# Kernel tuning notes

Hardware: AMD Instinct MI355X
Metric: run time of the kernel (lower is better)

The kernel has to match this reference:

```python
import jax, jax.numpy as jnp
import numpy as np

# FlowNetC correlation hyperparameters (from init_kwargs)
PAD = 20
KS = 1
MD = 20
S1 = 1
S2 = 2
MUL = 1


def setup_inputs() -> dict:
    key = jax.random.key(0)
    k1, k2 = jax.random.split(key)
    B, C, H, W = 8, 256, 96, 128
    input1 = jax.random.normal(k1, (B, C, H, W), dtype=jnp.float32)
    input2 = jax.random.normal(k2, (B, C, H, W), dtype=jnp.float32)
    return {"input1": input1, "input2": input2}


def _correlation(in1, in2):
    b, c, h, w = in1.shape
    p1 = jnp.pad(in1, ((0, 0), (0, 0), (PAD, PAD), (PAD, PAD)))
    p2 = jnp.pad(in2, ((0, 0), (0, 0), (PAD, PAD), (PAD, PAD)))
    hp, wp = h + 2 * PAD, w + 2 * PAD
    out_h = (hp - 2 * MD - KS) // S1 + 1
    out_w = (wp - 2 * MD - KS) // S1 + 1
    d = 2 * MD // S2 + 1  # number of displacement steps per axis (21)

    # fixed center region of input1: [b, c, out_h, out_w]
    region1 = p1[:, :, MD:MD + out_h * S1:S1, MD:MD + out_w * S1:S1]

    offs = (jnp.arange(d) - d // 2) * S2  # displacement offsets
    dys, dxs = jnp.meshgrid(offs, offs, indexing='ij')
    dys = dys.reshape(-1)
    dxs = dxs.reshape(-1)

    def step(carry, dydx):
        dy, dx = dydx
        y0 = MD + dy
        x0 = MD + dx
        valid = (y0 >= 0) & (x0 >= 0) & (y0 + out_h * S1 <= hp) & (x0 + out_w * S1 <= wp)
        reg2 = jax.lax.dynamic_slice(
            p2, (0, 0, y0, x0), (b, c, out_h * S1, out_w * S1)
        )[:, :, ::S1, ::S1]
        corr = (region1 * reg2).sum(axis=1) * MUL  # [b, out_h, out_w]
        corr = jnp.where(valid, corr, jnp.zeros_like(corr))
        return carry, corr

    _, chans = jax.lax.scan(step, None, (dys, dxs))  # [d*d, b, out_h, out_w]
    return jnp.transpose(chans, (1, 0, 2, 3))  # [b, d*d, out_h, out_w]


def reference(input1, input2):
    return _correlation(input1, input2)
```

## Files before the change

kernel.cpp:

```cpp
#include <hip/hip_runtime.h>
#include <stdint.h>

#define B_N   8
#define C_N   256
#define H_N   96
#define W_N   128
#define NCK   8
#define ND    21
#define NK    (ND * ND)

typedef __attribute__((ext_vector_type(8))) short short8;
typedef __attribute__((ext_vector_type(4))) float f32x4;

__device__ __forceinline__ uint32_t f2bf(float f) {
  uint32_t u = __builtin_bit_cast(uint32_t, f);
  return (u + 0x7fffu + ((u >> 16) & 1u)) >> 16;
}
__device__ __forceinline__ uint32_t packbf(float lo, float hi) {
  return f2bf(lo) | (f2bf(hi) << 16);
}
__device__ __forceinline__ void async16(void* lds_dst, const void* gsrc) {
  __builtin_amdgcn_global_load_lds(
      (const __attribute__((address_space(1))) void*)gsrc,
      (__attribute__((address_space(3))) void*)lds_dst, 16, 0, 0);
}

__global__ __launch_bounds__(256) void prep(const float* __restrict__ in1,
                                            const float* __restrict__ in2,
                                            unsigned short* __restrict__ Apre,
                                            unsigned short* __restrict__ Bpre) {
  __shared__ float tile[32][W_N + 1];
  int blk = blockIdx.x;
  bool isA = blk < 6144;
  int rblk = isA ? blk : blk - 6144;
  int ck = rblk & 7, bi = rblk >> 3;
  int b = bi / H_N, row = bi % H_N;
  const float* src = (isA ? in1 : in2) + ((size_t)(b * C_N + ck * 32) * H_N + row) * W_N;
  int tid = threadIdx.x;
  for (int idx = tid; idx < 32 * W_N; idx += 256) {
    int c = idx >> 7, j = idx & 127;
    tile[c][j] = src[(size_t)c * (H_N * W_N) + j];
  }
  __syncthreads();
  if (isA) {
    uint32_t* dst = (uint32_t*)Apre + (size_t)rblk * 2048;
    for (int q = tid; q < 2048; q += 256) {
      int e2 = q & 3, ln = (q >> 2) & 63, tp = q >> 8;
      int t = tp >> 1, p = tp & 1;
      int m = ln & 15, kg = ln >> 4;
      int c0 = kg * 8 + 2 * e2;
      int j = 32 * t + 2 * m + p;
      dst[q] = packbf(tile[c0][j], tile[c0 + 1][j]);
    }
  } else {
    uint32_t* dst = (uint32_t*)Bpre + (size_t)rblk * 3072;
    for (int q = tid; q < 3072; q += 256) {
      int e2 = q & 3, ln = (q >> 2) & 63, sp = q >> 8;
      int s = sp >> 1, p = sp & 1;
      int m = ln & 15, kg = ln >> 4;
      int c0 = kg * 8 + 2 * e2;
      int x = 32 * s + 2 * m - 20 + p;
      dst[q] = ((unsigned)x < 128u) ? packbf(tile[c0][x], tile[c0 + 1][x]) : 0u;
    }
  }
}

__global__ __launch_bounds__(768, 3) void corr_main(const unsigned short* __restrict__ Apre,
                                                    const unsigned short* __restrict__ Bpre,
                                                    float* __restrict__ out) {
  __shared__ __align__(16) char Bl[2][36864];

  int h = blockIdx.x;
  int b = h & 7, blk = h >> 3;
  int Y, pos;
  if (blk < 18)       { Y = blk - 20;                pos = 0; }
  else if (blk < 54)  { int t = blk - 18;  Y = -2 + (t >> 1); pos = t & 1; }
  else if (blk < 234) { int t = blk - 54;  Y = 16 + t / 3;    pos = t % 3; }
  else if (blk < 270) { int t = blk - 234; Y = 76 + (t >> 1); pos = t & 1; }
  else                { Y = 94 + (blk - 270);        pos = 0; }
  int g_min = (Y > 75) ? (Y - 70) / 6 : 0;
  int g_max = (Y + 20) / 6; if (g_max > 6) g_max = 6;

  int tid = threadIdx.x;
  int lane = tid & 63, w = tid >> 6;
  int rr = w >> 2, sub = w & 3;
  int p = sub & 1, th = sub >> 1;
  int m = lane & 15, kg = lane >> 4;

  int gidx = g_min + pos * 3 + rr;
  bool act = gidx <= g_max;
  int i_el = Y + 20 - 6 * gidx;
  int dyb = 3 * gidx;

  const char* bsrc[3];
  bool yval[3];
#pragma unroll
  for (int k = 0; k < 3; ++k) {
    int y = Y + 2 * k;
    yval[k] = (unsigned)y < (unsigned)H_N;
    bsrc[k] = (const char*)Bpre + (size_t)((b * H_N + (yval[k] ? y : 0)) * NCK) * 12288
              + w * 1024 + lane * 16;
  }
#pragma unroll
  for (int k = 0; k < 3; ++k) {
    if (!yval[k]) {
      short8 z = {};
      *(short8*)(&Bl[0][0] + k * 12288 + w * 1024 + lane * 16) = z;
      *(short8*)(&Bl[1][0] + k * 12288 + w * 1024 + lane * 16) = z;
    }
  }

  f32x4 acc[2][3][3];
#pragma unroll
  for (int a0i = 0; a0i < 2; ++a0i)
#pragma unroll
    for (int a1i = 0; a1i < 3; ++a1i)
#pragma unroll
      for (int a2i = 0; a2i < 3; ++a2i) acc[a0i][a1i][a2i] = {0.f, 0.f, 0.f, 0.f};

  const char* Ap = (const char*)Apre + (size_t)(b * H_N + (act ? i_el : 0)) * 65536
                   + ((4 * th + p) << 10) + lane * 16;

#pragma unroll
  for (int k = 0; k < 3; ++k)
    if (yval[k]) async16(&Bl[0][0] + k * 12288 + w * 1024, bsrc[k]);
  __syncthreads();

  for (int ck = 0; ck < NCK; ++ck) {
    char* cur = &Bl[ck & 1][0];
    if (ck < NCK - 1) {
      char* nxt = &Bl[(ck + 1) & 1][0];
#pragma unroll
      for (int k = 0; k < 3; ++k)
        if (yval[k]) async16(nxt + k * 12288 + w * 1024, bsrc[k] + (size_t)(ck + 1) * 12288);
    }
    if (act) {
      short8 a0 = *(const short8*)(Ap);
      short8 a1 = *(const short8*)(Ap + 2048);
#pragma unroll
      for (int ss = 0; ss < 4; ++ss) {
        int s = 2 * th + ss;
#pragma unroll
        for (int g = 0; g < 3; ++g) {
          short8 bbv = *(const short8*)(cur + g * 12288 + ((2 * s + p) << 10) + lane * 16);
          if (ss <= 2) acc[0][g][ss]     = __builtin_amdgcn_mfma_f32_16x16x32_bf16(a0, bbv, acc[0][g][ss], 0, 0, 0);
          if (ss >= 1) acc[1][g][ss - 1] = __builtin_amdgcn_mfma_f32_16x16x32_bf16(a1, bbv, acc[1][g][ss - 1], 0, 0, 0);
        }
      }
    }
    Ap += 8192;
    __syncthreads();
  }

  float* outl = (float*)(&Bl[0][0] + rr * 11072);
  int gt = sub * 64 + lane;
#pragma unroll
  for (int g = 0; g < 3; ++g) {
    if (act) {
#pragma unroll
      for (int tt = 0; tt < 2; ++tt) {
        int t = 2 * th + tt;
#pragma unroll
        for (int dl = 0; dl < 3; ++dl) {
#pragma unroll
          for (int r = 0; r < 4; ++r) {
            int a_ = kg * 4 + r;
            int dxi = 16 * dl + m - a_;
            if (dxi >= 0 && dxi <= 20) {
              int j = 2 * (16 * t + a_) + p;
              outl[dxi * 129 + j] = acc[tt][g][dl][r];
            }
          }
        }
      }
    }
    __syncthreads();
    if (act) {
      int dyi = dyb + g;
      size_t obase = ((size_t)(b * NK + dyi * ND) * H_N + i_el) * W_N;
      for (int idx = gt; idx < ND * W_N; idx += 256) {
        int dxi = idx >> 7, j = idx & 127;
        out[obase + (size_t)dxi * (H_N * W_N) + j] = outl[dxi * 129 + j];
      }
    }
    __syncthreads();
  }
}

__global__ void corr_naive(const float* __restrict__ in1, const float* __restrict__ in2,
                           float* __restrict__ out) {
  size_t o = (size_t)blockIdx.x * 256 + threadIdx.x;
  const size_t total = (size_t)B_N * NK * H_N * W_N;
  if (o >= total) return;
  int j = o & 127;
  int i = (int)((o >> 7) % H_N);
  int k = (int)((o / ((size_t)H_N * W_N)) % NK);
  int b = (int)(o / ((size_t)NK * H_N * W_N));
  int dyi = k / ND, dxi = k % ND;
  int y = i + 2 * dyi - 20, x = j + 2 * dxi - 20;
  float s = 0.f;
  if ((unsigned)y < (unsigned)H_N && (unsigned)x < (unsigned)W_N) {
    const float* p1 = in1 + ((size_t)b * C_N * H_N + i) * W_N + j;
    const float* p2 = in2 + ((size_t)b * C_N * H_N + y) * W_N + x;
    for (int c = 0; c < C_N; ++c)
      s += p1[(size_t)c * H_N * W_N] * p2[(size_t)c * H_N * W_N];
  }
  out[o] = s;
}

extern "C" void kernel_launch(void* const* d_in, const int* in_sizes, int n_in,
                              void* d_out, int out_size, void* d_ws, size_t ws_size,
                              hipStream_t stream) {
  const float* in1 = (const float*)d_in[0];
  const float* in2 = (const float*)d_in[1];
  float* out = (float*)d_out;

  const size_t A_BYTES = (size_t)6144 * 8192;
  const size_t B_BYTES = (size_t)6144 * 12288;
  if (ws_size < A_BYTES + B_BYTES) {
    size_t total = (size_t)B_N * NK * H_N * W_N;
    corr_naive<<<(int)((total + 255) / 256), 256, 0, stream>>>(in1, in2, out);
    return;
  }
  unsigned short* Apre = (unsigned short*)d_ws;
  unsigned short* Bpre = (unsigned short*)((char*)d_ws + A_BYTES);

  prep<<<12288, 256, 0, stream>>>(in1, in2, Apre, Bpre);
  corr_main<<<2304, 768, 0, stream>>>(Apre, Bpre, out);
}
```

Baseline: 200.4 us.

## Restructure correlation main loop into manually pipelined register/LDS double-buffered schedule

Rewrites the channel-chunk loop of corr_main as a fully unrolled software pipeline. A and edge B fragments are loaded straight into registers one chunk ahead, and only the 6 shared inner B units per row are staged in LDS through async loads. Explicit vmcnt waits, sched_barriers and raw s_barriers replace __syncthreads. This is meant to shrink the LDS footprint and overlap global loads with MFMA work, at the cost of more registers and fragile hand-written wait counts.

```diff
diff --git a/kernel.cpp b/kernel.cpp
--- a/kernel.cpp
+++ b/kernel.cpp
@@ -65,10 +65,60 @@
   }
 }
 
+#define MF(a, b, c) __builtin_amdgcn_mfma_f32_16x16x32_bf16(a, b, c, 0, 0, 0)
+#define SB0() __builtin_amdgcn_sched_barrier(0)
+#define BAR() __builtin_amdgcn_s_barrier()
+#define WAITV7() asm volatile("s_waitcnt vmcnt(7)" ::: "memory")
+#define WAITV0() asm volatile("s_waitcnt vmcnt(0)" ::: "memory")
+
+#define MF6(A0, A1, S0, S1, S2, S3, GI) do {                    \
+  acc[0][GI][0] = MF(A0, S0, acc[0][GI][0]);                    \
+  acc[0][GI][1] = MF(A0, S1, acc[0][GI][1]);                    \
+  acc[1][GI][0] = MF(A1, S1, acc[1][GI][0]);                    \
+  acc[0][GI][2] = MF(A0, S2, acc[0][GI][2]);                    \
+  acc[1][GI][1] = MF(A1, S2, acc[1][GI][1]);                    \
+  acc[1][GI][2] = MF(A1, S3, acc[1][GI][2]);                    \
+} while (0)
+
+#define ISSUE(AV0, AV1, GV0, GV1, GV2, CK) do {                                   \
+  async16(lds + (((CK) & 1) ? dst0b1 : dst0b0), src0 + (size_t)(CK) * 12288);     \
+  async16(lds + (((CK) & 1) ? dst1b1 : dst1b0), src1 + (size_t)(CK) * 12288);     \
+  AV0 = *(const short8*)(Ap + (size_t)(CK) * 8192);                               \
+  AV1 = *(const short8*)(Ap + (size_t)(CK) * 8192 + 2048);                        \
+  GV0 = *(const short8*)(bg0 + (size_t)(CK) * 12288);                             \
+  GV1 = *(const short8*)(bg1 + (size_t)(CK) * 12288);                             \
+  GV2 = *(const short8*)(bg2 + (size_t)(CK) * 12288);                             \
+} while (0)
+
+#define COMPG(AV0, AV1, GV, YV, GI, CK) do {                                      \
+  const char* cb_ = lds + ((CK) & 1) * 24576 + dsb + (GI) * 8192;                 \
+  short8 q0 = *(const short8*)(cb_);                                              \
+  short8 q1 = *(const short8*)(cb_ + 2048);                                       \
+  short8 q2 = *(const short8*)(cb_ + 4096);                                       \
+  short8 eg = (YV) ? (GV) : z8;                                                   \
+  if (th == 0) { MF6(AV0, AV1, eg, q0, q1, q2, GI); }                             \
+  else         { MF6(AV0, AV1, q0, q1, q2, eg, GI); }                             \
+} while (0)
+
+#define COMP(AV0, AV1, GV0, GV1, GV2, CK) do {                                    \
+  if (act) {                                                                      \
+    COMPG(AV0, AV1, GV0, yv0, 0, CK);                                             \
+    COMPG(AV0, AV1, GV1, yv1, 1, CK);                                             \
+    COMPG(AV0, AV1, GV2, yv2, 2, CK);                                             \
+  }                                                                               \
+} while (0)
+
+#define STEPK(IA0, IA1, IG0, IG1, IG2, KN, CA0, CA1, CG0, CG1, CG2, KC) do {      \
+  ISSUE(IA0, IA1, IG0, IG1, IG2, KN);                                             \
+  SB0(); WAITV7(); SB0(); BAR(); SB0();                                           \
+  COMP(CA0, CA1, CG0, CG1, CG2, KC);                                              \
+  SB0(); BAR(); SB0();                                                            \
+} while (0)
+
 __global__ __launch_bounds__(768, 3) void corr_main(const unsigned short* __restrict__ Apre,
                                                     const unsigned short* __restrict__ Bpre,
                                                     float* __restrict__ out) {
-  __shared__ __align__(16) char Bl[2][36864];
+  __shared__ __align__(16) char lds[50176];
 
   int h = blockIdx.x;
   int b = h & 7, blk = h >> 3;
@@ -92,67 +142,78 @@
   int i_el = Y + 20 - 6 * gidx;
   int dyb = 3 * gidx;
 
-  const char* bsrc[3];
-  bool yval[3];
-#pragma unroll
-  for (int k = 0; k < 3; ++k) {
-    int y = Y + 2 * k;
-    yval[k] = (unsigned)y < (unsigned)H_N;
-    bsrc[k] = (const char*)Bpre + (size_t)((b * H_N + (yval[k] ? y : 0)) * NCK) * 12288
-              + w * 1024 + lane * 16;
-  }
-#pragma unroll
-  for (int k = 0; k < 3; ++k) {
-    if (!yval[k]) {
-      short8 z = {};
-      *(short8*)(&Bl[0][0] + k * 12288 + w * 1024 + lane * 16) = z;
-      *(short8*)(&Bl[1][0] + k * 12288 + w * 1024 + lane * 16) = z;
-    }
-  }
-
-  f32x4 acc[2][3][3];
-#pragma unroll
-  for (int a0i = 0; a0i < 2; ++a0i)
-#pragma unroll
-    for (int a1i = 0; a1i < 3; ++a1i)
-#pragma unroll
-      for (int a2i = 0; a2i < 3; ++a2i) acc[a0i][a1i][a2i] = {0.f, 0.f, 0.f, 0.f};
+  bool yv0, yv1, yv2;
+  const char* brow_s[3];
+  {
+    bool yv[3];
+#pragma unroll
+    for (int g = 0; g < 3; ++g) {
+      int y = Y + 2 * g;
+      yv[g] = (unsigned)y < (unsigned)H_N;
+      brow_s[g] = (const char*)Bpre + (size_t)((b * H_N + (yv[g] ? y : 0)) * NCK) * 12288;
+    }
+    yv0 = yv[0]; yv1 = yv[1]; yv2 = yv[2];
+  }
+
+  int f0 = 2 * w, f1 = 2 * w + 1;
+  int g0 = f0 >> 3, u0 = f0 & 7, g1 = f1 >> 3, u1 = f1 & 7;
+  bool v0 = (g0 == 0) ? yv0 : (g0 == 1) ? yv1 : yv2;
+  bool v1 = (g1 == 0) ? yv0 : (g1 == 1) ? yv1 : yv2;
+  int dst0b0 = v0 ? (g0 * 8192 + u0 * 1024 + lane * 16) : (49152 + lane * 16);
+  int dst0b1 = v0 ? (dst0b0 + 24576) : dst0b0;
+  int dst1b0 = v1 ? (g1 * 8192 + u1 * 1024 + lane * 16) : (49152 + lane * 16);
+  int dst1b1 = v1 ? (dst1b0 + 24576) : dst1b0;
+  const char* src0 = brow_s[g0] + 2048 + u0 * 1024 + lane * 16;
+  const char* src1 = brow_s[g1] + 2048 + u1 * 1024 + lane * 16;
 
   const char* Ap = (const char*)Apre + (size_t)(b * H_N + (act ? i_el : 0)) * 65536
                    + ((4 * th + p) << 10) + lane * 16;
-
-#pragma unroll
-  for (int k = 0; k < 3; ++k)
-    if (yval[k]) async16(&Bl[0][0] + k * 12288 + w * 1024, bsrc[k]);
-  __syncthreads();
-
-  for (int ck = 0; ck < NCK; ++ck) {
-    char* cur = &Bl[ck & 1][0];
-    if (ck < NCK - 1) {
-      char* nxt = &Bl[(ck + 1) & 1][0];
-#pragma unroll
-      for (int k = 0; k < 3; ++k)
-        if (yval[k]) async16(nxt + k * 12288 + w * 1024, bsrc[k] + (size_t)(ck + 1) * 12288);
-    }
-    if (act) {
-      short8 a0 = *(const short8*)(Ap);
-      short8 a1 = *(const short8*)(Ap + 2048);
-#pragma unroll
-      for (int ss = 0; ss < 4; ++ss) {
-        int s = 2 * th + ss;
-#pragma unroll
-        for (int g = 0; g < 3; ++g) {
-          short8 bbv = *(const short8*)(cur + g * 12288 + ((2 * s + p) << 10) + lane * 16);
-          if (ss <= 2) acc[0][g][ss]     = __builtin_amdgcn_mfma_f32_16x16x32_bf16(a0, bbv, acc[0][g][ss], 0, 0, 0);
-          if (ss >= 1) acc[1][g][ss - 1] = __builtin_amdgcn_mfma_f32_16x16x32_bf16(a1, bbv, acc[1][g][ss - 1], 0, 0, 0);
+  int gunit = (th ? 10 : 0) + p;
+  const char* bg0 = brow_s[0] + gunit * 1024 + lane * 16;
+  const char* bg1 = brow_s[1] + gunit * 1024 + lane * 16;
+  const char* bg2 = brow_s[2] + gunit * 1024 + lane * 16;
+
+  int dsb = (p + (th ? 2 : 0)) * 1024 + lane * 16;
+
+  f32x4 acc[2][3][3];
+#pragma unroll
+  for (int a0i = 0; a0i < 2; ++a0i)
+#pragma unroll
+    for (int a1i = 0; a1i < 3; ++a1i)
+#pragma unroll
+      for (int a2i = 0; a2i < 3; ++a2i) acc[a0i][a1i][a2i] = {0.f, 0.f, 0.f, 0.f};
+
+  short8 z8 = {};
+
+  {
+    bool yv[3] = {yv0, yv1, yv2};
+#pragma unroll
+    for (int g = 0; g < 3; ++g) {
+      if (!yv[g]) {
+        for (int idx = tid; idx < 1024; idx += 768) {
+          int bs = idx >> 9, of = (idx & 511) * 16;
+          *(short8*)(lds + bs * 24576 + g * 8192 + of) = z8;
         }
       }
     }
-    Ap += 8192;
-    __syncthreads();
-  }
-
-  float* outl = (float*)(&Bl[0][0] + rr * 11072);
+  }
+  asm volatile("s_waitcnt lgkmcnt(0)" ::: "memory");
+
+  short8 aP0, aP1, gP0, gP1, gP2, aQ0, aQ1, gQ0, gQ1, gQ2;
+
+  ISSUE(aP0, aP1, gP0, gP1, gP2, 0);
+  STEPK(aQ0, aQ1, gQ0, gQ1, gQ2, 1, aP0, aP1, gP0, gP1, gP2, 0);
+  STEPK(aP0, aP1, gP0, gP1, gP2, 2, aQ0, aQ1, gQ0, gQ1, gQ2, 1);
+  STEPK(aQ0, aQ1, gQ0, gQ1, gQ2, 3, aP0, aP1, gP0, gP1, gP2, 2);
+  STEPK(aP0, aP1, gP0, gP1, gP2, 4, aQ0, aQ1, gQ0, gQ1, gQ2, 3);
+  STEPK(aQ0, aQ1, gQ0, gQ1, gQ2, 5, aP0, aP1, gP0, gP1, gP2, 4);
+  STEPK(aP0, aP1, gP0, gP1, gP2, 6, aQ0, aQ1, gQ0, gQ1, gQ2, 5);
+  STEPK(aQ0, aQ1, gQ0, gQ1, gQ2, 7, aP0, aP1, gP0, gP1, gP2, 6);
+  WAITV0(); SB0(); BAR(); SB0();
+  COMP(aQ0, aQ1, gQ0, gQ1, gQ2, 7);
+  __syncthreads();
+
+  float* outl = (float*)(lds + rr * 11072);
   int gt = sub * 64 + lane;
 #pragma unroll
   for (int g = 0; g < 3; ++g) {
```

Measured after the change: 214.1 us. 1.07x slower.

## Stage A through LDS, pipeline with split barriers, and rebalance MFMA tiles across waves

Applied to the files above, without the earlier changes.

The A operand is now staged into LDS with async global-to-LDS loads alongside B, so each block issues one unified stream of prefetches per channel chunk. The chunk loop is manually unrolled with explicit vmcnt waits and raw s_barriers so the next stage's loads are issued right after compute. The work split also changes: each wave computes 6 MFMA tiles per displacement group, a triangular set chosen by swapping operand order for the second half, replacing the previous 2x3 layout that included wasted tiles. The cost is a much larger LDS footprint (~121 KB), which likely cuts occupancy, plus more complex, harder-to-verify indexing.

```diff
diff --git a/kernel.cpp b/kernel.cpp
--- a/kernel.cpp
+++ b/kernel.cpp
@@ -65,10 +65,55 @@
   }
 }
 
+#define MF(a, b, c) __builtin_amdgcn_mfma_f32_16x16x32_bf16(a, b, c, 0, 0, 0)
+
+#define STAGE(CK, BUF) do {                                                       \
+  _Pragma("unroll")                                                               \
+  for (int r_ = 0; r_ < 5; ++r_)                                                  \
+    async16(lds + ((BUF) ? fdst1[r_] : fdst0[r_]),                                \
+            fsrc[r_] + (size_t)(CK) * fstr[r_]);                                  \
+} while (0)
+
+#define CHUNK(CK, BUFOFF, VN, DOSTAGE, STCK, STBUF) do {                          \
+  asm volatile("s_waitcnt vmcnt(" #VN ")" ::: "memory");                          \
+  __builtin_amdgcn_s_barrier();                                                   \
+  __builtin_amdgcn_sched_barrier(0);                                              \
+  if (act) {                                                                      \
+    const char* bc_ = lds + (BUFOFF);                                             \
+    short8 a0 = *(const short8*)(bc_ + aoff);                                     \
+    short8 a1 = *(const short8*)(bc_ + aoff + 2048);                              \
+    short8 a2 = *(const short8*)(bc_ + aoff + 4096);                              \
+    _Pragma("unroll")                                                             \
+    for (int g_ = 0; g_ < 3; ++g_) {                                              \
+      const char* bb_ = bc_ + boff + g_ * 12288;                                  \
+      short8 b0 = *(const short8*)(bb_);                                          \
+      short8 b1 = *(const short8*)(bb_ + 2048);                                   \
+      short8 b2 = *(const short8*)(bb_ + 4096);                                   \
+      if (th == 0) {        \
+        acc[g_][0] = MF(a0, b0, acc[g_][0]);                                      \
+        acc[g_][1] = MF(a0, b1, acc[g_][1]);                                      \
+        acc[g_][2] = MF(a1, b1, acc[g_][2]);                                      \
+        acc[g_][3] = MF(a0, b2, acc[g_][3]);                                      \
+        acc[g_][4] = MF(a1, b2, acc[g_][4]);                                      \
+        acc[g_][5] = MF(a2, b2, acc[g_][5]);                                      \
+      } else {         \
+        acc[g_][0] = MF(b0, a0, acc[g_][0]);                                      \
+        acc[g_][1] = MF(b0, a1, acc[g_][1]);                                      \
+        acc[g_][2] = MF(b1, a1, acc[g_][2]);                                      \
+        acc[g_][3] = MF(b0, a2, acc[g_][3]);                                      \
+        acc[g_][4] = MF(b1, a2, acc[g_][4]);                                      \
+        acc[g_][5] = MF(b2, a2, acc[g_][5]);                                      \
+      }                                                                           \
+    }                                                                             \
+  }                                                                               \
+  __builtin_amdgcn_s_barrier();                                                   \
+  if (DOSTAGE) STAGE(STCK, STBUF);                                                \
+} while (0)
+
 __global__ __launch_bounds__(768, 3) void corr_main(const unsigned short* __restrict__ Apre,
                                                     const unsigned short* __restrict__ Bpre,
                                                     float* __restrict__ out) {
-  __shared__ __align__(16) char Bl[2][36864];
+  __shared__ __align__(16) char lds[123904];
 
   int h = blockIdx.x;
   int b = h & 7, blk = h >> 3;
@@ -83,93 +128,92 @@
 
   int tid = threadIdx.x;
   int lane = tid & 63, w = tid >> 6;
-  int rr = w >> 2, sub = w & 3;
+  int el = w >> 2, sub = w & 3;
   int p = sub & 1, th = sub >> 1;
   int m = lane & 15, kg = lane >> 4;
 
-  int gidx = g_min + pos * 3 + rr;
+  int gidx = g_min + pos * 3 + el;
   bool act = gidx <= g_max;
   int i_el = Y + 20 - 6 * gidx;
   int dyb = 3 * gidx;
 
-  const char* bsrc[3];
-  bool yval[3];
-#pragma unroll
-  for (int k = 0; k < 3; ++k) {
-    int y = Y + 2 * k;
-    yval[k] = (unsigned)y < (unsigned)H_N;
-    bsrc[k] = (const char*)Bpre + (size_t)((b * H_N + (yval[k] ? y : 0)) * NCK) * 12288
-              + w * 1024 + lane * 16;
-  }
-#pragma unroll
-  for (int k = 0; k < 3; ++k) {
-    if (!yval[k]) {
-      short8 z = {};
-      *(short8*)(&Bl[0][0] + k * 12288 + w * 1024 + lane * 16) = z;
-      *(short8*)(&Bl[1][0] + k * 12288 + w * 1024 + lane * 16) = z;
-    }
-  }
-
-  f32x4 acc[2][3][3];
-#pragma unroll
-  for (int a0i = 0; a0i < 2; ++a0i)
-#pragma unroll
-    for (int a1i = 0; a1i < 3; ++a1i)
-#pragma unroll
-      for (int a2i = 0; a2i < 3; ++a2i) acc[a0i][a1i][a2i] = {0.f, 0.f, 0.f, 0.f};
-
-  const char* Ap = (const char*)Apre + (size_t)(b * H_N + (act ? i_el : 0)) * 65536
-                   + ((4 * th + p) << 10) + lane * 16;
-
-#pragma unroll
-  for (int k = 0; k < 3; ++k)
-    if (yval[k]) async16(&Bl[0][0] + k * 12288 + w * 1024, bsrc[k]);
+  int fdst0[5], fdst1[5], fstr[5];
+  const char* fsrc[5];
+#pragma unroll
+  for (int r = 0; r < 5; ++r) {
+    int u = w * 5 + r;
+    if (u < 24) {
+      int ael = u >> 3, tp = u & 7;
+      int gi = g_min + pos * 3 + ael;
+      int ia = Y + 20 - 6 * gi; ia = ia < 0 ? 0 : (ia > 95 ? 95 : ia);
+      int dst = ael * 8192 + tp * 1024 + lane * 16;
+      fdst0[r] = dst; fdst1[r] = dst + 61440;
+      fsrc[r] = (const char*)Apre + ((size_t)(b * H_N + ia) * NCK) * 8192 + tp * 1024 + lane * 16;
+      fstr[r] = 8192;
+    } else {
+      int v = u - 24, k = v / 12, sp = v - k * 12;
+      int y = Y + 2 * k;
+      bool vy = (unsigned)y < (unsigned)H_N;
+      int dst = vy ? (24576 + k * 12288 + sp * 1024 + lane * 16) : (122880 + lane * 16);
+      fdst0[r] = dst; fdst1[r] = vy ? (dst + 61440) : dst;
+      fsrc[r] = (const char*)Bpre + ((size_t)(b * H_N + (vy ? y : 0)) * NCK) * 12288
+                + sp * 1024 + lane * 16;
+      fstr[r] = 12288;
+    }
+  }
+
+  {
+    short8 z = {};
+#pragma unroll
+    for (int k = 0; k < 3; ++k) {
+      int y = Y + 2 * k;
+      if ((unsigned)y >= (unsigned)H_N) {
+        *(short8*)(lds + 24576 + k * 12288 + tid * 16) = z;
+        *(short8*)(lds + 61440 + 24576 + k * 12288 + tid * 16) = z;
+      }
+    }
+  }
+  asm volatile("s_waitcnt lgkmcnt(0)" ::: "memory");
+
+  f32x4 acc[3][6];
+#pragma unroll
+  for (int gi = 0; gi < 3; ++gi)
+#pragma unroll
+    for (int ki = 0; ki < 6; ++ki) acc[gi][ki] = {0.f, 0.f, 0.f, 0.f};
+
+  int aoff = el * 8192 + th * 2048 + p * 1024 + lane * 16;
+  int boff = 24576 + th * 6144 + p * 1024 + lane * 16;
+
+  STAGE(0, 0);
+  STAGE(1, 1);
+  CHUNK(0, 0,     5, 1, 2, 0);
+  CHUNK(1, 61440, 5, 1, 3, 1);
+  CHUNK(2, 0,     5, 1, 4, 0);
+  CHUNK(3, 61440, 5, 1, 5, 1);
+  CHUNK(4, 0,     5, 1, 6, 0);
+  CHUNK(5, 61440, 5, 1, 7, 1);
+  CHUNK(6, 0,     5, 0, 0, 0);
+  CHUNK(7, 61440, 0, 0, 0, 0);
   __syncthreads();
 
-  for (int ck = 0; ck < NCK; ++ck) {
-    char* cur = &Bl[ck & 1][0];
-    if (ck < NCK - 1) {
-      char* nxt = &Bl[(ck + 1) & 1][0];
-#pragma unroll
-      for (int k = 0; k < 3; ++k)
-        if (yval[k]) async16(nxt + k * 12288 + w * 1024, bsrc[k] + (size_t)(ck + 1) * 12288);
-    }
-    if (act) {
-      short8 a0 = *(const short8*)(Ap);
-      short8 a1 = *(const short8*)(Ap + 2048);
-#pragma unroll
-      for (int ss = 0; ss < 4; ++ss) {
-        int s = 2 * th + ss;
-#pragma unroll
-        for (int g = 0; g < 3; ++g) {
-          short8 bbv = *(const short8*)(cur + g * 12288 + ((2 * s + p) << 10) + lane * 16);
-          if (ss <= 2) acc[0][g][ss]     = __builtin_amdgcn_mfma_f32_16x16x32_bf16(a0, bbv, acc[0][g][ss], 0, 0, 0);
-          if (ss >= 1) acc[1][g][ss - 1] = __builtin_amdgcn_mfma_f32_16x16x32_bf16(a1, bbv, acc[1][g][ss - 1], 0, 0, 0);
-        }
-      }
-    }
-    Ap += 8192;
-    __syncthreads();
-  }
-
-  float* outl = (float*)(&Bl[0][0] + rr * 11072);
+  float* outl = (float*)(lds + el * 11072);
   int gt = sub * 64 + lane;
 #pragma unroll
   for (int g = 0; g < 3; ++g) {
     if (act) {
 #pragma unroll
-      for (int tt = 0; tt < 2; ++tt) {
-        int t = 2 * th + tt;
-#pragma unroll
-        for (int dl = 0; dl < 3; ++dl) {
-#pragma unroll
-          for (int r = 0; r < 4; ++r) {
-            int a_ = kg * 4 + r;
-            int dxi = 16 * dl + m - a_;
-            if (dxi >= 0 && dxi <= 20) {
-              int j = 2 * (16 * t + a_) + p;
-              outl[dxi * 129 + j] = acc[tt][g][dl][r];
-            }
+      for (int k = 0; k < 6; ++k) {
+        const int T0c[6] = {0, 0, 1, 0, 1, 2}, S0c[6] = {0, 1, 1, 2, 2, 2};
+        const int T1c[6] = {1, 2, 2, 3, 3, 3}, S1c[6] = {3, 3, 4, 3, 4, 5};
+        int T = th ? T1c[k] : T0c[k];
+        int S = th ? S1c[k] : S0c[k];
+#pragma unroll
+        for (int r = 0; r < 4; ++r) {
+          int a_ = kg * 4 + r;
+          int dxi = 16 * (S - T) + (th ? (a_ - m) : (m - a_));
+          if (dxi >= 0 && dxi <= 20) {
+            int j = 2 * (16 * T + (th ? m : a_)) + p;
+            outl[dxi * 129 + j] = acc[g][k][r];
           }
         }
       }
```

Result: slower. 209.6 us (+4.6%).
